# Performance work log

Hardware: AMD Instinct MI355X
Metric: run time of the kernel (lower is better)

## Reference

```python
import jax, jax.numpy as jnp
import numpy as np

B, C, H, W, N_REF = 4, 256, 128, 128, 4


def setup_inputs() -> dict:
    key = jax.random.key(0)
    ks = jax.random.split(key, 9)
    s = 1.0 / np.sqrt(C)
    x = jax.random.normal(ks[0], (B, C, H, W), jnp.float32)
    Wq = jax.random.normal(ks[1], (C, C), jnp.float32) * s
    bq = jax.random.normal(ks[2], (C,), jnp.float32) * 0.01
    Wk = jax.random.normal(ks[3], (C, C), jnp.float32) * s
    bk = jax.random.normal(ks[4], (C,), jnp.float32) * 0.01
    Wv = jax.random.normal(ks[5], (C, C), jnp.float32) * s
    bv = jax.random.normal(ks[6], (C,), jnp.float32) * 0.01
    Wo = jax.random.normal(ks[7], (2 * N_REF, C), jnp.float32) * s
    bo = jax.random.normal(ks[8], (2 * N_REF,), jnp.float32) * 0.01
    return {"x": x, "Wq": Wq, "bq": bq, "Wk": Wk, "bk": bk,
            "Wv": Wv, "bv": bv, "Wo": Wo, "bo": bo}


def _proj(Wt, bt, x):
    # 1x1 conv == per-pixel channel matmul
    return jnp.einsum('oc,bchw->bohw', Wt, x) + bt[None, :, None, None]


def reference(x, Wq, bq, Wk, bk, Wv, bv, Wo, bo):
    b, c, h, w = x.shape
    n = Wo.shape[0] // 2
    hw = h * w

    Q = _proj(Wq, bq, x)
    K = _proj(Wk, bk, x)
    V = _proj(Wv, bv, x)

    offsets = _proj(Wo, bo, Q).reshape(b, n, 2, h, w)

    grid_w = jnp.arange(w, dtype=jnp.float32)[None, None, None, :]
    grid_h = jnp.arange(h, dtype=jnp.float32)[None, None, :, None]
    # clamp then truncate toward zero (matches torch .clamp().long() for >=0 values)
    ref_w = jnp.clip(grid_w + offsets[:, :, 0], 0, w - 1)
    ref_h = jnp.clip(grid_h + offsets[:, :, 1], 0, h - 1)
    idx = (jax.lax.stop_gradient(ref_h).astype(jnp.int32) * w
           + jax.lax.stop_gradient(ref_w).astype(jnp.int32)).reshape(b, n * hw)

    K_flat = K.reshape(b, c, hw)
    V_flat = V.reshape(b, c, hw)
    Kg = jnp.take_along_axis(K_flat, idx[:, None, :], axis=2).reshape(b, c, n, hw)
    Vg = jnp.take_along_axis(V_flat, idx[:, None, :], axis=2).reshape(b, c, n, hw)

    Q_flat = Q.reshape(b, c, hw)
    # NOTE: original module applies no softmax/scale — raw dot-product weights
    attn = jnp.einsum('bch,bcnh->bnh', Q_flat, Kg)
    out = jnp.einsum('bnh,bcnh->bch', attn, Vg)
    return out.reshape(b, c, h, w)
```

## Files before the change

kernel.cpp:

```cpp
#include <hip/hip_runtime.h>

#define HW   16384
#define CH   256
#define WD   128
#define NPTS 4

typedef _Float16 half8 __attribute__((ext_vector_type(8)));
typedef _Float16 half4 __attribute__((ext_vector_type(4)));
typedef float    f32x4 __attribute__((ext_vector_type(4)));

#define WS_XT    0ull
#define WS_WQK   33554432ull
#define WS_WV    33685504ull
#define WS_WOQ   33816576ull
#define WS_BOF   33824768ull
#define WS_CVEC  33824832ull
#define WS_DVEC  33825856ull
#define WS_SC    33826880ull
#define WS_SVEC  33826944ull
#define WS_IDX   34089088ull

__global__ void k_wprep(const float* __restrict__ Wq, const float* __restrict__ bq,
                        const float* __restrict__ Wk, const float* __restrict__ bk,
                        const float* __restrict__ Wv, const float* __restrict__ bv,
                        const float* __restrict__ Wo, const float* __restrict__ bo,
                        _Float16* __restrict__ wqk16, float* __restrict__ cvec,
                        _Float16* __restrict__ wv16, float* __restrict__ woq,
                        float* __restrict__ bof, float* __restrict__ dvec,
                        float* __restrict__ scst) {
    int bid = blockIdx.x, t = threadIdx.x;
    if (bid < 256) {
        int i = bid;
        float s = 0.f;
        for (int o = 0; o < 256; o++) s += Wk[o * 256 + i] * Wq[o * 256 + t];
        wqk16[i * 256 + t] = (_Float16)s;
        if (t == 0) {
            float cs = 0.f;
            for (int o = 0; o < 256; o++) cs += Wk[o * 256 + i] * bq[o];
            cvec[i] = cs;
        }
    } else if (bid < 512) {
        int r = bid - 256;
        wv16[r * 256 + t] = (_Float16)Wv[r * 256 + t];
    } else if (bid < 520) {
        int j = bid - 512;
        float s = 0.f;
        for (int o = 0; o < 256; o++) s += Wo[j * 256 + o] * Wq[o * 256 + t];
        woq[t * 8 + j] = s;
        if (t == 0) {
            float tt = bo[j];
            for (int o = 0; o < 256; o++) tt += Wo[j * 256 + o] * bq[o];
            bof[j] = tt;
        }
    } else {
        float s = 0.f;
        for (int o = 0; o < 256; o++) s += bk[o] * Wq[o * 256 + t];
        dvec[t] = s;
        if (t == 0) {
            float sc = 0.f;
            for (int o = 0; o < 256; o++) sc += bq[o] * bk[o];
            scst[0] = sc;
        }
    }
}

__launch_bounds__(256)
__global__ void k_prep(const float* __restrict__ x, const float* __restrict__ woq,
                       const float* __restrict__ bof, const float* __restrict__ dvec,
                       const float* __restrict__ scst,
                       _Float16* __restrict__ xt, int* __restrict__ idxb,
                       float* __restrict__ svec) {
    __shared__ float    wl[256 * 8];
    __shared__ float    dl[256];
    __shared__ float    bl8[8];
    __shared__ _Float16 tile[64][280];
    __shared__ float    red[4][64][8];
    __shared__ float    reds[4][64];

    int t = threadIdx.x;
    for (int i = t; i < 256 * 8; i += 256) wl[i] = woq[i];
    dl[t] = dvec[t];
    if (t < 8) bl8[t] = bof[t];
    __syncthreads();

    int b = blockIdx.y;
    int p0 = blockIdx.x * 64;
    int pl = t & 63, cg = t >> 6;
    const float* xb = x + (size_t)b * CH * HW + p0 + pl;

    float acc[8];
    #pragma unroll
    for (int j = 0; j < 8; j++) acc[j] = 0.f;
    float accs = 0.f;

    for (int i0 = 0; i0 < 64; i0 += 8) {
        half8 hv;
        #pragma unroll
        for (int i = 0; i < 8; i++) {
            int c = cg * 64 + i0 + i;
            float xv = xb[(size_t)c * HW];
            hv[i] = (_Float16)xv;
            accs += dl[c] * xv;
            #pragma unroll
            for (int j = 0; j < 8; j++) acc[j] += wl[c * 8 + j] * xv;
        }
        *(half8*)(&tile[pl][cg * 64 + i0]) = hv;
    }
    #pragma unroll
    for (int j = 0; j < 8; j++) red[cg][pl][j] = acc[j];
    reds[cg][pl] = accs;
    __syncthreads();

    {
        int n = cg, p = p0 + pl;
        float sw_ = bl8[2 * n]     + red[0][pl][2 * n]     + red[1][pl][2 * n]
                                   + red[2][pl][2 * n]     + red[3][pl][2 * n];
        float sh_ = bl8[2 * n + 1] + red[0][pl][2 * n + 1] + red[1][pl][2 * n + 1]
                                   + red[2][pl][2 * n + 1] + red[3][pl][2 * n + 1];
        int h = p >> 7, w = p & 127;
        float rw = fminf(fmaxf((float)w + sw_, 0.f), 127.f);
        float rh = fminf(fmaxf((float)h + sh_, 0.f), 127.f);
        idxb[(b * NPTS + n) * HW + p] = ((int)rh) * WD + (int)rw;
        if (cg == 0)
            svec[b * HW + p] = reds[0][pl] + reds[1][pl] + reds[2][pl] + reds[3][pl] + scst[0];
    }

    {
        int row = t >> 2;
        size_t gbase = ((size_t)(b * HW + p0 + row)) * 256;
        #pragma unroll
        for (int s = 0; s < 8; s++) {
            int seg = (t & 3) + s * 4;
            *(uint4*)(xt + gbase + seg * 8) = *(const uint4*)(&tile[row][seg * 8]);
        }
    }
}

__launch_bounds__(256)
__global__ void k_fused(const _Float16* __restrict__ xt, const _Float16* __restrict__ wqk16,
                        const _Float16* __restrict__ wv16, const float* __restrict__ cvec,
                        const float* __restrict__ bv, const int* __restrict__ idxb,
                        const float* __restrict__ svec, float* __restrict__ out) {
    __shared__ _Float16 QW[128 * 256];
    __shared__ _Float16 As[128 * 32];
    __shared__ _Float16 Bs[128 * 32];

    int tid = threadIdx.x;
    int b = blockIdx.y;
    int bx = blockIdx.x;
    int logical = (bx & 7) * 16 + (bx >> 3);
    int p0 = logical * 128;
    size_t mrow0 = (size_t)b * HW + p0;

    int lane = tid & 63, wid = tid >> 6;
    int wr = wid >> 1, wc = wid & 1;
    int g = lane >> 4, r = lane & 15;
    int ar = tid >> 2, aseg = tid & 3;
    int sw = aseg ^ ((ar >> 1) & 3);

    for (int nh = 0; nh < 2; nh++) {
        f32x4 acc[4][4] = {};
        for (int kt = 0; kt < 8; kt++) {
            int k0 = kt * 32;
            uint4 a0 = *(const uint4*)(xt + (mrow0 + ar) * 256 + k0 + aseg * 8);
            uint4 a1 = *(const uint4*)(xt + (mrow0 + 64 + ar) * 256 + k0 + aseg * 8);
            uint4 b0 = *(const uint4*)(wqk16 + (size_t)(nh * 128 + ar) * 256 + k0 + aseg * 8);
            uint4 b1 = *(const uint4*)(wqk16 + (size_t)(nh * 128 + 64 + ar) * 256 + k0 + aseg * 8);
            __syncthreads();
            *(uint4*)(As + ar * 32 + sw * 8)        = a0;
            *(uint4*)(As + (64 + ar) * 32 + sw * 8) = a1;
            *(uint4*)(Bs + ar * 32 + sw * 8)        = b0;
            *(uint4*)(Bs + (64 + ar) * 32 + sw * 8) = b1;
            __syncthreads();

            half8 af[4], bf[4];
            #pragma unroll
            for (int mb = 0; mb < 4; mb++) {
                int row = wr * 64 + mb * 16 + r;
                int slot = g ^ ((row >> 1) & 3);
                af[mb] = *(const half8*)(As + row * 32 + slot * 8);
            }
            #pragma unroll
            for (int nb = 0; nb < 4; nb++) {
                int row = wc * 64 + nb * 16 + r;
                int slot = g ^ ((row >> 1) & 3);
                bf[nb] = *(const half8*)(Bs + row * 32 + slot * 8);
            }
            #pragma unroll
            for (int mb = 0; mb < 4; mb++)
                #pragma unroll
                for (int nb = 0; nb < 4; nb++)
                    acc[mb][nb] = __builtin_amdgcn_mfma_f32_16x16x32_f16(bf[nb], af[mb], acc[mb][nb], 0, 0, 0);
        }
        #pragma unroll
        for (int mb = 0; mb < 4; mb++) {
            int row = wr * 64 + mb * 16 + r;
            #pragma unroll
            for (int nb = 0; nb < 4; nb++) {
                int ncol = nh * 128 + wc * 64 + nb * 16 + g * 4;
                f32x4 cv = *(const f32x4*)(cvec + ncol);
                half4 h;
                #pragma unroll
                for (int i = 0; i < 4; i++) h[i] = (_Float16)(acc[mb][nb][i] + cv[i]);
                *(half4*)(&QW[(row << 8) + (ncol ^ ((row & 7) << 3))]) = h;
            }
        }
    }
    __syncthreads();

    {
        float* asf = (float*)As;
        int seg = tid & 15, pslot = tid >> 4;
        for (int it = 0; it < 8; it++) {
            int pl = it * 16 + pslot;
            size_t m = mrow0 + pl;
            int qa0 = (pl << 8) + ((seg * 16)     ^ ((pl & 7) << 3));
            int qa1 = (pl << 8) + ((seg * 16 + 8) ^ ((pl & 7) << 3));
            half8 q0 = *(const half8*)(&QW[qa0]);
            half8 q1 = *(const half8*)(&QW[qa1]);
            float sv = svec[m];
            int jj[NPTS];
            #pragma unroll
            for (int n = 0; n < NPTS; n++) jj[n] = idxb[(b * NPTS + n) * HW + p0 + pl];

            half8 xv[NPTS][2];
            #pragma unroll
            for (int n = 0; n < NPTS; n++) {
                const half8* xr = (const half8*)(xt + ((size_t)b * HW + jj[n]) * 256 + seg * 16);
                xv[n][0] = xr[0];
                xv[n][1] = xr[1];
            }
            float o[16];
            #pragma unroll
            for (int e = 0; e < 16; e++) o[e] = 0.f;
            float asl = 0.f;
            #pragma unroll
            for (int n = 0; n < NPTS; n++) {
                float d = 0.f;
                #pragma unroll
                for (int e = 0; e < 8; e++) d += (float)q0[e] * (float)xv[n][0][e];
                #pragma unroll
                for (int e = 0; e < 8; e++) d += (float)q1[e] * (float)xv[n][1][e];
                d += __shfl_xor(d, 1);
                d += __shfl_xor(d, 2);
                d += __shfl_xor(d, 4);
                d += __shfl_xor(d, 8);
                float a = d + sv;
                asl += a;
                #pragma unroll
                for (int e = 0; e < 8; e++) o[e]     += a * (float)xv[n][0][e];
                #pragma unroll
                for (int e = 0; e < 8; e++) o[8 + e] += a * (float)xv[n][1][e];
            }
            half8 h0, h1;
            #pragma unroll
            for (int e = 0; e < 8; e++) { h0[e] = (_Float16)o[e]; h1[e] = (_Float16)o[8 + e]; }
            *(half8*)(&QW[qa0]) = h0;
            *(half8*)(&QW[qa1]) = h1;
            if (seg == 0) asf[pl] = asl;
        }
    }
    __syncthreads();

    {
        const float* asf = (const float*)As;
        for (int nh = 0; nh < 2; nh++) {
            f32x4 acc[4][4] = {};
            for (int kt = 0; kt < 8; kt++) {
                int k0 = kt * 32;
                uint4 b0 = *(const uint4*)(wv16 + (size_t)(nh * 128 + ar) * 256 + k0 + aseg * 8);
                uint4 b1 = *(const uint4*)(wv16 + (size_t)(nh * 128 + 64 + ar) * 256 + k0 + aseg * 8);
                __syncthreads();
                *(uint4*)(Bs + ar * 32 + sw * 8)        = b0;
                *(uint4*)(Bs + (64 + ar) * 32 + sw * 8) = b1;
                __syncthreads();

                half8 af[4], bf[4];
                #pragma unroll
                for (int mb = 0; mb < 4; mb++) {
                    int row = wr * 64 + mb * 16 + r;
                    af[mb] = *(const half8*)(&QW[(row << 8) + ((k0 + g * 8) ^ ((row & 7) << 3))]);
                }
                #pragma unroll
                for (int nb = 0; nb < 4; nb++) {
                    int row = wc * 64 + nb * 16 + r;
                    int slot = g ^ ((row >> 1) & 3);
                    bf[nb] = *(const half8*)(Bs + row * 32 + slot * 8);
                }
                #pragma unroll
                for (int mb = 0; mb < 4; mb++)
                    #pragma unroll
                    for (int nb = 0; nb < 4; nb++)
                        acc[mb][nb] = __builtin_amdgcn_mfma_f32_16x16x32_f16(bf[nb], af[mb], acc[mb][nb], 0, 0, 0);
            }
            #pragma unroll
            for (int mb = 0; mb < 4; mb++) {
                int mrow = wr * 64 + mb * 16 + r;
                float am = asf[mrow];
                float* obase = out + (size_t)b * CH * HW + p0 + mrow;
                #pragma unroll
                for (int nb = 0; nb < 4; nb++) {
                    int cb = nh * 128 + wc * 64 + nb * 16 + g * 4;
                    f32x4 bb = *(const f32x4*)(bv + cb);
                    #pragma unroll
                    for (int i = 0; i < 4; i++)
                        obase[(size_t)(cb + i) * HW] = acc[mb][nb][i] + am * bb[i];
                }
            }
        }
    }
}

extern "C" void kernel_launch(void* const* d_in, const int* in_sizes, int n_in,
                              void* d_out, int out_size, void* d_ws, size_t ws_size,
                              hipStream_t stream) {
    const float* x  = (const float*)d_in[0];
    const float* Wq = (const float*)d_in[1];
    const float* bq = (const float*)d_in[2];
    const float* Wk = (const float*)d_in[3];
    const float* bk = (const float*)d_in[4];
    const float* Wv = (const float*)d_in[5];
    const float* bv = (const float*)d_in[6];
    const float* Wo = (const float*)d_in[7];
    const float* bo = (const float*)d_in[8];
    (void)in_sizes; (void)n_in; (void)out_size; (void)ws_size;

    char* ws = (char*)d_ws;
    _Float16* xt    = (_Float16*)(ws + WS_XT);
    _Float16* wqk16 = (_Float16*)(ws + WS_WQK);
    _Float16* wv16  = (_Float16*)(ws + WS_WV);
    float*    woq   = (float*)(ws + WS_WOQ);
    float*    bof   = (float*)(ws + WS_BOF);
    float*    cvec  = (float*)(ws + WS_CVEC);
    float*    dvec  = (float*)(ws + WS_DVEC);
    float*    scst  = (float*)(ws + WS_SC);
    float*    svec  = (float*)(ws + WS_SVEC);
    int*      idxb  = (int*)(ws + WS_IDX);

    k_wprep<<<521, 256, 0, stream>>>(Wq, bq, Wk, bk, Wv, bv, Wo, bo,
                                     wqk16, cvec, wv16, woq, bof, dvec, scst);
    k_prep<<<dim3(256, 4), 256, 0, stream>>>(x, woq, bof, dvec, scst, xt, idxb, svec);
    k_fused<<<dim3(128, 4), 256, 0, stream>>>(xt, wqk16, wv16, cvec, bv, idxb, svec,
                                              (float*)d_out);
}
```

Baseline: 91.37 us.

## Halve fused tile to 64 pixels, load MFMA operands directly with register prefetch

The fused kernel now processes 64 pixels per block instead of 128, with twice as many blocks, and shrinks shared memory to a 64x256 QW buffer so more blocks fit per CU (launch bounds ask for 4). The GEMM stages drop the LDS staging tiles and their two barriers per k-step. Each wave instead loads its MFMA fragments straight from global memory, with one k-step of register double-buffering. The gather stage's per-thread channel split changes to two 8-wide halves. The trade-off is more redundant global or L2 reads of the weights across blocks and less register-level reuse per block.

```diff
diff --git a/kernel.cpp b/kernel.cpp
--- a/kernel.cpp
+++ b/kernel.cpp
@@ -136,65 +136,57 @@
     }
 }
 
-__launch_bounds__(256)
+__launch_bounds__(256, 4)
 __global__ void k_fused(const _Float16* __restrict__ xt, const _Float16* __restrict__ wqk16,
                         const _Float16* __restrict__ wv16, const float* __restrict__ cvec,
                         const float* __restrict__ bv, const int* __restrict__ idxb,
                         const float* __restrict__ svec, float* __restrict__ out) {
-    __shared__ _Float16 QW[128 * 256];
-    __shared__ _Float16 As[128 * 32];
-    __shared__ _Float16 Bs[128 * 32];
+    __shared__ _Float16 QW[64 * 256];
+    __shared__ float    asf[64];
 
     int tid = threadIdx.x;
     int b = blockIdx.y;
     int bx = blockIdx.x;
-    int logical = (bx & 7) * 16 + (bx >> 3);
-    int p0 = logical * 128;
+    int logical = (bx & 7) * 32 + (bx >> 3);
+    int p0 = logical * 64;
     size_t mrow0 = (size_t)b * HW + p0;
 
     int lane = tid & 63, wid = tid >> 6;
     int wr = wid >> 1, wc = wid & 1;
     int g = lane >> 4, r = lane & 15;
-    int ar = tid >> 2, aseg = tid & 3;
-    int sw = aseg ^ ((ar >> 1) & 3);
-
+
+    #pragma unroll 1
     for (int nh = 0; nh < 2; nh++) {
-        f32x4 acc[4][4] = {};
+        const _Float16* Ap = xt + (mrow0 + wr * 32 + r) * 256 + g * 8;
+        const _Float16* Bp = wqk16 + (size_t)(nh * 128 + wc * 64 + r) * 256 + g * 8;
+        f32x4 acc[2][4] = {};
+        half8 afc[2], bfc[4], afn[2], bfn[4];
+        #pragma unroll
+        for (int mb = 0; mb < 2; mb++) afc[mb] = *(const half8*)(Ap + mb * 16 * 256);
+        #pragma unroll
+        for (int nb = 0; nb < 4; nb++) bfc[nb] = *(const half8*)(Bp + nb * 16 * 256);
         for (int kt = 0; kt < 8; kt++) {
-            int k0 = kt * 32;
-            uint4 a0 = *(const uint4*)(xt + (mrow0 + ar) * 256 + k0 + aseg * 8);
-            uint4 a1 = *(const uint4*)(xt + (mrow0 + 64 + ar) * 256 + k0 + aseg * 8);
-            uint4 b0 = *(const uint4*)(wqk16 + (size_t)(nh * 128 + ar) * 256 + k0 + aseg * 8);
-            uint4 b1 = *(const uint4*)(wqk16 + (size_t)(nh * 128 + 64 + ar) * 256 + k0 + aseg * 8);
-            __syncthreads();
-            *(uint4*)(As + ar * 32 + sw * 8)        = a0;
-            *(uint4*)(As + (64 + ar) * 32 + sw * 8) = a1;
-            *(uint4*)(Bs + ar * 32 + sw * 8)        = b0;
-            *(uint4*)(Bs + (64 + ar) * 32 + sw * 8) = b1;
-            __syncthreads();
-
-            half8 af[4], bf[4];
-            #pragma unroll
-            for (int mb = 0; mb < 4; mb++) {
-                int row = wr * 64 + mb * 16 + r;
-                int slot = g ^ ((row >> 1) & 3);
-                af[mb] = *(const half8*)(As + row * 32 + slot * 8);
-            }
-            #pragma unroll
-            for (int nb = 0; nb < 4; nb++) {
-                int row = wc * 64 + nb * 16 + r;
-                int slot = g ^ ((row >> 1) & 3);
-                bf[nb] = *(const half8*)(Bs + row * 32 + slot * 8);
-            }
-            #pragma unroll
-            for (int mb = 0; mb < 4; mb++)
+            if (kt < 7) {
+                #pragma unroll
+                for (int mb = 0; mb < 2; mb++)
+                    afn[mb] = *(const half8*)(Ap + mb * 16 * 256 + (kt + 1) * 32);
                 #pragma unroll
                 for (int nb = 0; nb < 4; nb++)
-                    acc[mb][nb] = __builtin_amdgcn_mfma_f32_16x16x32_f16(bf[nb], af[mb], acc[mb][nb], 0, 0, 0);
-        }
-        #pragma unroll
-        for (int mb = 0; mb < 4; mb++) {
-            int row = wr * 64 + mb * 16 + r;
+                    bfn[nb] = *(const half8*)(Bp + nb * 16 * 256 + (kt + 1) * 32);
+            }
+            #pragma unroll
+            for (int mb = 0; mb < 2; mb++)
+                #pragma unroll
+                for (int nb = 0; nb < 4; nb++)
+                    acc[mb][nb] = __builtin_amdgcn_mfma_f32_16x16x32_f16(bfc[nb], afc[mb], acc[mb][nb], 0, 0, 0);
+            #pragma unroll
+            for (int mb = 0; mb < 2; mb++) afc[mb] = afn[mb];
+            #pragma unroll
+            for (int nb = 0; nb < 4; nb++) bfc[nb] = bfn[nb];
+        }
+        #pragma unroll
+        for (int mb = 0; mb < 2; mb++) {
+            int row = wr * 32 + mb * 16 + r;
             #pragma unroll
             for (int nb = 0; nb < 4; nb++) {
                 int ncol = nh * 128 + wc * 64 + nb * 16 + g * 4;
@@ -209,13 +201,13 @@
     __syncthreads();
 
     {
-        float* asf = (float*)As;
         int seg = tid & 15, pslot = tid >> 4;
-        for (int it = 0; it < 8; it++) {
+        #pragma unroll 1
+        for (int it = 0; it < 4; it++) {
             int pl = it * 16 + pslot;
             size_t m = mrow0 + pl;
-            int qa0 = (pl << 8) + ((seg * 16)     ^ ((pl & 7) << 3));
-            int qa1 = (pl << 8) + ((seg * 16 + 8) ^ ((pl & 7) << 3));
+            int qa0 = (pl << 8) + ((seg * 8)       ^ ((pl & 7) << 3));
+            int qa1 = (pl << 8) + ((128 + seg * 8) ^ ((pl & 7) << 3));
             half8 q0 = *(const half8*)(&QW[qa0]);
             half8 q1 = *(const half8*)(&QW[qa1]);
             float sv = svec[m];
@@ -223,24 +215,24 @@
             #pragma unroll
             for (int n = 0; n < NPTS; n++) jj[n] = idxb[(b * NPTS + n) * HW + p0 + pl];
 
-            half8 xv[NPTS][2];
+            half8 xv0[NPTS], xv1[NPTS];
             #pragma unroll
             for (int n = 0; n < NPTS; n++) {
-                const half8* xr = (const half8*)(xt + ((size_t)b * HW + jj[n]) * 256 + seg * 16);
-                xv[n][0] = xr[0];
-                xv[n][1] = xr[1];
-            }
-            float o[16];
-            #pragma unroll
-            for (int e = 0; e < 16; e++) o[e] = 0.f;
+                const _Float16* xr = xt + ((size_t)b * HW + jj[n]) * 256;
+                xv0[n] = *(const half8*)(xr + seg * 8);
+                xv1[n] = *(const half8*)(xr + 128 + seg * 8);
+            }
+            float o0[8], o1[8];
+            #pragma unroll
+            for (int e = 0; e < 8; e++) { o0[e] = 0.f; o1[e] = 0.f; }
             float asl = 0.f;
             #pragma unroll
             for (int n = 0; n < NPTS; n++) {
                 float d = 0.f;
                 #pragma unroll
-                for (int e = 0; e < 8; e++) d += (float)q0[e] * (float)xv[n][0][e];
-                #pragma unroll
-                for (int e = 0; e < 8; e++) d += (float)q1[e] * (float)xv[n][1][e];
+                for (int e = 0; e < 8; e++) d += (float)q0[e] * (float)xv0[n][e];
+                #pragma unroll
+                for (int e = 0; e < 8; e++) d += (float)q1[e] * (float)xv1[n][e];
                 d += __shfl_xor(d, 1);
                 d += __shfl_xor(d, 2);
                 d += __shfl_xor(d, 4);
@@ -248,13 +240,13 @@
                 float a = d + sv;
                 asl += a;
                 #pragma unroll
-                for (int e = 0; e < 8; e++) o[e]     += a * (float)xv[n][0][e];
-                #pragma unroll
-                for (int e = 0; e < 8; e++) o[8 + e] += a * (float)xv[n][1][e];
+                for (int e = 0; e < 8; e++) o0[e] += a * (float)xv0[n][e];
+                #pragma unroll
+                for (int e = 0; e < 8; e++) o1[e] += a * (float)xv1[n][e];
             }
             half8 h0, h1;
             #pragma unroll
-            for (int e = 0; e < 8; e++) { h0[e] = (_Float16)o[e]; h1[e] = (_Float16)o[8 + e]; }
+            for (int e = 0; e < 8; e++) { h0[e] = (_Float16)o0[e]; h1[e] = (_Float16)o1[e]; }
             *(half8*)(&QW[qa0]) = h0;
             *(half8*)(&QW[qa1]) = h1;
             if (seg == 0) asf[pl] = asl;
@@ -262,50 +254,45 @@
     }
     __syncthreads();
 
-    {
-        const float* asf = (const float*)As;
-        for (int nh = 0; nh < 2; nh++) {
-            f32x4 acc[4][4] = {};
-            for (int kt = 0; kt < 8; kt++) {
-                int k0 = kt * 32;
-                uint4 b0 = *(const uint4*)(wv16 + (size_t)(nh * 128 + ar) * 256 + k0 + aseg * 8);
-                uint4 b1 = *(const uint4*)(wv16 + (size_t)(nh * 128 + 64 + ar) * 256 + k0 + aseg * 8);
-                __syncthreads();
-                *(uint4*)(Bs + ar * 32 + sw * 8)        = b0;
-                *(uint4*)(Bs + (64 + ar) * 32 + sw * 8) = b1;
-                __syncthreads();
-
-                half8 af[4], bf[4];
-                #pragma unroll
-                for (int mb = 0; mb < 4; mb++) {
-                    int row = wr * 64 + mb * 16 + r;
-                    af[mb] = *(const half8*)(&QW[(row << 8) + ((k0 + g * 8) ^ ((row & 7) << 3))]);
-                }
-                #pragma unroll
-                for (int nb = 0; nb < 4; nb++) {
-                    int row = wc * 64 + nb * 16 + r;
-                    int slot = g ^ ((row >> 1) & 3);
-                    bf[nb] = *(const half8*)(Bs + row * 32 + slot * 8);
-                }
-                #pragma unroll
-                for (int mb = 0; mb < 4; mb++)
-                    #pragma unroll
-                    for (int nb = 0; nb < 4; nb++)
-                        acc[mb][nb] = __builtin_amdgcn_mfma_f32_16x16x32_f16(bf[nb], af[mb], acc[mb][nb], 0, 0, 0);
-            }
-            #pragma unroll
-            for (int mb = 0; mb < 4; mb++) {
-                int mrow = wr * 64 + mb * 16 + r;
-                float am = asf[mrow];
-                float* obase = out + (size_t)b * CH * HW + p0 + mrow;
-                #pragma unroll
-                for (int nb = 0; nb < 4; nb++) {
-                    int cb = nh * 128 + wc * 64 + nb * 16 + g * 4;
-                    f32x4 bb = *(const f32x4*)(bv + cb);
-                    #pragma unroll
-                    for (int i = 0; i < 4; i++)
-                        obase[(size_t)(cb + i) * HW] = acc[mb][nb][i] + am * bb[i];
-                }
+    #pragma unroll 1
+    for (int nh = 0; nh < 2; nh++) {
+        const _Float16* Bp = wv16 + (size_t)(nh * 128 + wc * 64 + r) * 256 + g * 8;
+        f32x4 acc[2][4] = {};
+        half8 bfc[4], bfn[4];
+        #pragma unroll
+        for (int nb = 0; nb < 4; nb++) bfc[nb] = *(const half8*)(Bp + nb * 16 * 256);
+        for (int kt = 0; kt < 8; kt++) {
+            if (kt < 7) {
+                #pragma unroll
+                for (int nb = 0; nb < 4; nb++)
+                    bfn[nb] = *(const half8*)(Bp + nb * 16 * 256 + (kt + 1) * 32);
+            }
+            half8 af[2];
+            #pragma unroll
+            for (int mb = 0; mb < 2; mb++) {
+                int row = wr * 32 + mb * 16 + r;
+                af[mb] = *(const half8*)(&QW[(row << 8) + ((kt * 32 + g * 8) ^ ((row & 7) << 3))]);
+            }
+            #pragma unroll
+            for (int mb = 0; mb < 2; mb++)
+                #pragma unroll
+                for (int nb = 0; nb < 4; nb++)
+                    acc[mb][nb] = __builtin_amdgcn_mfma_f32_16x16x32_f16(bfc[nb], af[mb], acc[mb][nb], 0, 0, 0);
+            #pragma unroll
+            for (int nb = 0; nb < 4; nb++) bfc[nb] = bfn[nb];
+        }
+        #pragma unroll
+        for (int mb = 0; mb < 2; mb++) {
+            int mrow = wr * 32 + mb * 16 + r;
+            float am = asf[mrow];
+            float* obase = out + (size_t)b * CH * HW + p0 + mrow;
+            #pragma unroll
+            for (int nb = 0; nb < 4; nb++) {
+                int cb = nh * 128 + wc * 64 + nb * 16 + g * 4;
+                f32x4 bb = *(const f32x4*)(bv + cb);
+                #pragma unroll
+                for (int i = 0; i < 4; i++)
+                    obase[(size_t)(cb + i) * HW] = acc[mb][nb][i] + am * bb[i];
             }
         }
     }
@@ -340,6 +327,6 @@
     k_wprep<<<521, 256, 0, stream>>>(Wq, bq, Wk, bk, Wv, bv, Wo, bo,
                                      wqk16, cvec, wv16, woq, bof, dvec, scst);
     k_prep<<<dim3(256, 4), 256, 0, stream>>>(x, woq, bof, dvec, scst, xt, idxb, svec);
-    k_fused<<<dim3(128, 4), 256, 0, stream>>>(xt, wqk16, wv16, cvec, bv, idxb, svec,
+    k_fused<<<dim3(256, 4), 256, 0, stream>>>(xt, wqk16, wv16, cvec, bv, idxb, svec,
                                               (float*)d_out);
 }
```

After: 130.1 us. +42.4%, slower.
